# Kernel tuning notes

Measured on AMD Instinct MI355X. Metric: run time of the kernel, lower is better.

The kernel has to match this reference:

```python
import jax, jax.numpy as jnp
import numpy as np

T = 100          # number of landscape sample points
K_MAX = 2        # landscape depth
GRID = (256, 256)
N = GRID[0] * GRID[1]
B = 256          # batch size
P = 1024         # persistence pairs per sample (from the cubical complex)
DIMENSIONS = (0, 1)
BIG = jnp.float32(1e30)  # finite sentinel instead of inf (avoids inf arithmetic)


def setup_inputs() -> dict:
    key = jax.random.key(0)
    k1, k2, k3, k4 = jax.random.split(key, 4)
    inputs = jax.random.uniform(k1, (B, N), dtype=jnp.float32)
    dim_idx = jax.random.randint(k2, (B, P), 0, 2, dtype=jnp.int32)
    b_loc = jax.random.randint(k3, (B, P), 0, N, dtype=jnp.int32)
    d_loc = jax.random.randint(k4, (B, P), 0, N, dtype=jnp.int32)
    # persistence pairs satisfy death value >= birth value; swap to honor that
    vb = jnp.take_along_axis(inputs, b_loc, axis=1)
    vd = jnp.take_along_axis(inputs, d_loc, axis=1)
    swap = vb > vd
    birth_loc = jnp.where(swap, d_loc, b_loc)
    death_loc = jnp.where(swap, b_loc, d_loc)
    return {"inputs": inputs, "dim_idx": dim_idx,
            "birth_loc": birth_loc, "death_loc": death_loc}


def _landscape_sample(dtm, dim_idx, b_loc, d_loc):
    # dtm: [N] filtration values; pairs: [P] each
    births = dtm[b_loc]  # [P] birth value = input at birth cell
    deaths = dtm[d_loc]  # [P]
    lands, trange = [], []
    for dim in DIMENSIONS:
        valid = dim_idx == dim                     # [P] pairs of this homology dim
        count = jnp.sum(valid)
        # robust t-range: first K_MAX valid pairs in given (lexsort) order
        rank = jnp.cumsum(valid.astype(jnp.int32)) - 1
        sel = valid & (rank < K_MAX)
        t_min = jnp.min(jnp.where(sel, births, BIG))
        t_max = jnp.max(jnp.where(sel, deaths, -BIG))
        t_min = jnp.where(count > 0, t_min, 0.0)
        t_max = jnp.where(count > 0, t_max, 0.0)
        # original custom grad does NOT differentiate through tseq
        tseq = jax.lax.stop_gradient(jnp.linspace(t_min, t_max, T))  # [T]
        b = jnp.where(valid, births, BIG)
        d = jnp.where(valid, deaths, -BIG)
        # tent functions: [T, P]
        fab = jnp.maximum(jnp.minimum(tseq[:, None] - b[None, :],
                                      d[None, :] - tseq[:, None]), 0.0)
        land, _ = jax.lax.top_k(fab, K_MAX)        # == -sort(-fab)[:, :K_MAX]
        land = jnp.where(count > 0, land, jnp.zeros_like(land))
        nonzero = (count > 0) & (jnp.max(land) > 0)
        trange.append(jnp.where(nonzero, t_min, 0.0))
        trange.append(jnp.where(nonzero, t_max, 0.0))
        lands.append(land)
    return jnp.stack(lands), jax.lax.stop_gradient(jnp.stack(trange))


def reference(inputs, dim_idx, birth_loc, death_loc):
    # landscape: [B, len(DIMENSIONS), T, K_MAX]; t_range: [B, 2*len(DIMENSIONS)]
    land, t_range = jax.vmap(_landscape_sample)(inputs, dim_idx, birth_loc, death_loc)
    return land, t_range
```

## Files before the change

### kernel.cpp

```cpp
#include <hip/hip_runtime.h>

#define TT 100
#define PP 1024
#define NN 65536
#define BIGV 1e30f

__global__ __launch_bounds__(1024) void adpl_kernel(
    const float* __restrict__ inputs,
    const int*   __restrict__ dim_idx,
    const int*   __restrict__ birth_loc,
    const int*   __restrict__ death_loc,
    float*       __restrict__ out_land,
    float*       __restrict__ out_trange)
{
    __shared__ float2 bd[2][PP];
    __shared__ unsigned long long s_mask[16];
    __shared__ float  s_tmin[2], s_tmax[2];
    __shared__ int    s_count[2];
    __shared__ int    s_maxland[2];
    __shared__ float2 s_part[2][TT][4];

    const int b   = blockIdx.x;
    const int tid = threadIdx.x;

    if (tid < 2) s_maxland[tid] = 0;

    {
        const int p  = tid;
        const int di = dim_idx [(size_t)b * PP + p];
        const int bl = birth_loc[(size_t)b * PP + p];
        const int dl = death_loc[(size_t)b * PP + p];
        const float bv = inputs[(size_t)b * NN + bl];
        const float dv = inputs[(size_t)b * NN + dl];
        const bool v0 = (di == 0);
        bd[0][p] = v0 ? make_float2(bv, dv) : make_float2(BIGV, -BIGV);
        bd[1][p] = v0 ? make_float2(BIGV, -BIGV) : make_float2(bv, dv);
        const unsigned long long m0 = __ballot(v0);
        if ((tid & 63) == 0) s_mask[tid >> 6] = m0;
    }
    __syncthreads();

    if (tid < 2) {
        const int d = tid;
        int cnt = 0, p1 = -1, p2 = -1;
        for (int w = 0; w < 16; w++) {
            unsigned long long m = (d == 0) ? s_mask[w] : ~s_mask[w];
            cnt += __popcll(m);
            if (p2 < 0 && m) {
                if (p1 < 0) {
                    p1 = w * 64 + __ffsll(m) - 1;
                    m &= m - 1;
                    if (m) p2 = w * 64 + __ffsll(m) - 1;
                } else {
                    p2 = w * 64 + __ffsll(m) - 1;
                }
            }
        }
        float tmin = 0.f, tmax = 0.f;
        if (cnt > 0) {
            const float2 e1 = bd[d][p1];
            tmin = e1.x; tmax = e1.y;
            if (cnt > 1) {
                const float2 e2 = bd[d][p2];
                tmin = fminf(tmin, e2.x);
                tmax = fmaxf(tmax, e2.y);
            }
        }
        s_tmin[d] = tmin; s_tmax[d] = tmax; s_count[d] = cnt;
    }
    __syncthreads();

    {
        const int d   = tid >> 9;
        const int idx = tid & 511;
        const int t   = idx >> 2;
        const int c   = idx & 3;
        if (t < TT) {
            const float tmin = s_tmin[d], tmax = s_tmax[d];
            const float step = (tmax - tmin) * (1.0f / (TT - 1));
            const float tv = (t == TT - 1) ? tmax : fmaf((float)t, step, tmin);
            float M1 = 0.f, M2 = 0.f;
            const float2* __restrict__ arr = bd[d];
            #pragma unroll 8
            for (int i = 0; i < 256; i++) {
                const float2 e = arr[4 * i + c];
                const float f = fminf(tv - e.x, e.y - tv);
                M2 = fmaxf(M2, fminf(M1, f));
                M1 = fmaxf(M1, f);
            }
            s_part[d][t][c] = make_float2(M1, M2);
        }
    }
    __syncthreads();

    if (tid < 256) {
        const int d2 = tid >> 7, t2 = tid & 127;
        if (t2 < TT) {
            float m1 = 0.f, m2 = 0.f;
            #pragma unroll
            for (int cc = 0; cc < 4; cc++) {
                const float2 pr = s_part[d2][t2][cc];
                m2 = fmaxf(m2, fminf(m1, pr.x));
                m1 = fmaxf(m1, pr.x);
                m2 = fmaxf(m2, pr.y);
            }
            const size_t base = ((size_t)(b * 2 + d2) * TT + t2) * 2;
            out_land[base + 0] = m1;
            out_land[base + 1] = m2;
            atomicMax(&s_maxland[d2], __float_as_int(m1));
        }
    }
    __syncthreads();

    if (tid < 2) {
        const int d = tid;
        const bool nz = (s_count[d] > 0) && (__int_as_float(s_maxland[d]) > 0.f);
        out_trange[(size_t)b * 4 + 2 * d + 0] = nz ? s_tmin[d] : 0.f;
        out_trange[(size_t)b * 4 + 2 * d + 1] = nz ? s_tmax[d] : 0.f;
    }
}

extern "C" void kernel_launch(void* const* d_in, const int* in_sizes, int n_in,
                              void* d_out, int out_size, void* d_ws, size_t ws_size,
                              hipStream_t stream) {
    const float* inputs    = (const float*)d_in[0];
    const int*   dim_idx   = (const int*)d_in[1];
    const int*   birth_loc = (const int*)d_in[2];
    const int*   death_loc = (const int*)d_in[3];

    const int B = in_sizes[1] / PP;

    float* out_land   = (float*)d_out;
    float* out_trange = out_land + (size_t)B * 2 * TT * 2;

    adpl_kernel<<<B, 1024, 0, stream>>>(inputs, dim_idx, birth_loc, death_loc,
                                        out_land, out_trange);
}
```

Before: 106.7 us.

## Split homology dimensions across a second grid axis with 8-way partial scans

Launches one block per (sample, dimension) instead of one block per sample, so each block stages only one dimension's pairs and scans 128 elements per thread with 8 partial lanes per sample point. This doubles the block count, giving more parallelism across the GPU's compute units, and halves per-thread serial work in the tent-function top-2 scan. In exchange, the gather of inputs and the index loads are repeated for both dimensions, and a launch-bounds occupancy hint is added. The partial-result buffer is padded to 9 lanes to reduce shared-memory bank conflicts.

```diff
diff --git a/kernel.cpp b/kernel.cpp
--- a/kernel.cpp
+++ b/kernel.cpp
@@ -5,7 +5,7 @@
 #define NN 65536
 #define BIGV 1e30f
 
-__global__ __launch_bounds__(1024) void adpl_kernel(
+__global__ __launch_bounds__(1024, 8) void adpl_kernel(
     const float* __restrict__ inputs,
     const int*   __restrict__ dim_idx,
     const int*   __restrict__ birth_loc,
@@ -13,17 +13,18 @@
     float*       __restrict__ out_land,
     float*       __restrict__ out_trange)
 {
-    __shared__ float2 bd[2][PP];
+    __shared__ float2 bd[PP];
     __shared__ unsigned long long s_mask[16];
-    __shared__ float  s_tmin[2], s_tmax[2];
-    __shared__ int    s_count[2];
-    __shared__ int    s_maxland[2];
-    __shared__ float2 s_part[2][TT][4];
+    __shared__ float  s_tmin, s_tmax;
+    __shared__ int    s_count;
+    __shared__ int    s_maxland;
+    __shared__ float2 s_part[TT][9];
 
     const int b   = blockIdx.x;
+    const int d   = blockIdx.y;
     const int tid = threadIdx.x;
 
-    if (tid < 2) s_maxland[tid] = 0;
+    if (tid == 0) s_maxland = 0;
 
     {
         const int p  = tid;
@@ -32,19 +33,17 @@
         const int dl = death_loc[(size_t)b * PP + p];
         const float bv = inputs[(size_t)b * NN + bl];
         const float dv = inputs[(size_t)b * NN + dl];
-        const bool v0 = (di == 0);
-        bd[0][p] = v0 ? make_float2(bv, dv) : make_float2(BIGV, -BIGV);
-        bd[1][p] = v0 ? make_float2(BIGV, -BIGV) : make_float2(bv, dv);
-        const unsigned long long m0 = __ballot(v0);
-        if ((tid & 63) == 0) s_mask[tid >> 6] = m0;
+        const bool v = (di == d);
+        bd[p] = v ? make_float2(bv, dv) : make_float2(BIGV, -BIGV);
+        const unsigned long long m = __ballot(v);
+        if ((tid & 63) == 0) s_mask[tid >> 6] = m;
     }
     __syncthreads();
 
-    if (tid < 2) {
-        const int d = tid;
+    if (tid == 0) {
         int cnt = 0, p1 = -1, p2 = -1;
         for (int w = 0; w < 16; w++) {
-            unsigned long long m = (d == 0) ? s_mask[w] : ~s_mask[w];
+            unsigned long long m = s_mask[w];
             cnt += __popcll(m);
             if (p2 < 0 && m) {
                 if (p1 < 0) {
@@ -58,65 +57,59 @@
         }
         float tmin = 0.f, tmax = 0.f;
         if (cnt > 0) {
-            const float2 e1 = bd[d][p1];
+            const float2 e1 = bd[p1];
             tmin = e1.x; tmax = e1.y;
             if (cnt > 1) {
-                const float2 e2 = bd[d][p2];
+                const float2 e2 = bd[p2];
                 tmin = fminf(tmin, e2.x);
                 tmax = fmaxf(tmax, e2.y);
             }
         }
-        s_tmin[d] = tmin; s_tmax[d] = tmax; s_count[d] = cnt;
+        s_tmin = tmin; s_tmax = tmax; s_count = cnt;
     }
     __syncthreads();
 
     {
-        const int d   = tid >> 9;
-        const int idx = tid & 511;
-        const int t   = idx >> 2;
-        const int c   = idx & 3;
+        const int t = tid >> 3;
+        const int c = tid & 7;
         if (t < TT) {
-            const float tmin = s_tmin[d], tmax = s_tmax[d];
+            const float tmin = s_tmin, tmax = s_tmax;
             const float step = (tmax - tmin) * (1.0f / (TT - 1));
             const float tv = (t == TT - 1) ? tmax : fmaf((float)t, step, tmin);
             float M1 = 0.f, M2 = 0.f;
-            const float2* __restrict__ arr = bd[d];
             #pragma unroll 8
-            for (int i = 0; i < 256; i++) {
-                const float2 e = arr[4 * i + c];
+            for (int i = 0; i < 128; i++) {
+                const float2 e = bd[8 * i + c];
                 const float f = fminf(tv - e.x, e.y - tv);
                 M2 = fmaxf(M2, fminf(M1, f));
                 M1 = fmaxf(M1, f);
             }
-            s_part[d][t][c] = make_float2(M1, M2);
+            s_part[t][c] = make_float2(M1, M2);
         }
     }
     __syncthreads();
 
-    if (tid < 256) {
-        const int d2 = tid >> 7, t2 = tid & 127;
-        if (t2 < TT) {
-            float m1 = 0.f, m2 = 0.f;
-            #pragma unroll
-            for (int cc = 0; cc < 4; cc++) {
-                const float2 pr = s_part[d2][t2][cc];
-                m2 = fmaxf(m2, fminf(m1, pr.x));
-                m1 = fmaxf(m1, pr.x);
-                m2 = fmaxf(m2, pr.y);
-            }
-            const size_t base = ((size_t)(b * 2 + d2) * TT + t2) * 2;
-            out_land[base + 0] = m1;
-            out_land[base + 1] = m2;
-            atomicMax(&s_maxland[d2], __float_as_int(m1));
+    if (tid < TT) {
+        const int t = tid;
+        float m1 = 0.f, m2 = 0.f;
+        #pragma unroll
+        for (int cc = 0; cc < 8; cc++) {
+            const float2 pr = s_part[t][cc];
+            m2 = fmaxf(m2, fminf(m1, pr.x));
+            m1 = fmaxf(m1, pr.x);
+            m2 = fmaxf(m2, pr.y);
         }
+        const size_t base = ((size_t)(b * 2 + d) * TT + t) * 2;
+        out_land[base + 0] = m1;
+        out_land[base + 1] = m2;
+        atomicMax(&s_maxland, __float_as_int(m1));
     }
     __syncthreads();
 
-    if (tid < 2) {
-        const int d = tid;
-        const bool nz = (s_count[d] > 0) && (__int_as_float(s_maxland[d]) > 0.f);
-        out_trange[(size_t)b * 4 + 2 * d + 0] = nz ? s_tmin[d] : 0.f;
-        out_trange[(size_t)b * 4 + 2 * d + 1] = nz ? s_tmax[d] : 0.f;
+    if (tid == 0) {
+        const bool nz = (s_count > 0) && (__int_as_float(s_maxland) > 0.f);
+        out_trange[(size_t)b * 4 + 2 * d + 0] = nz ? s_tmin : 0.f;
+        out_trange[(size_t)b * 4 + 2 * d + 1] = nz ? s_tmax : 0.f;
     }
 }
 
@@ -133,6 +126,7 @@
     float* out_land   = (float*)d_out;
     float* out_trange = out_land + (size_t)B * 2 * TT * 2;
 
-    adpl_kernel<<<B, 1024, 0, stream>>>(inputs, dim_idx, birth_loc, death_loc,
-                                        out_land, out_trange);
+    dim3 grid(B, 2);
+    adpl_kernel<<<grid, 1024, 0, stream>>>(inputs, dim_idx, birth_loc, death_loc,
+                                           out_land, out_trange);
 }
```

After: 105.4 us. No clear change (-1.3%).
